# Optimization experiments

Hardware: AMD Instinct MI355X
Metric: run time of the kernel (lower is better)

## Reference

```python
import jax, jax.numpy as jnp
import numpy as np

N_USER = 50000
N_ITEM = 50000
E = 600000
D = 128
H = 2 * D  # FFN hidden
LN_EPS = 1e-5


def _xavier(k, shape):
    lim = float(np.sqrt(6.0 / (shape[0] + shape[1])))
    return jax.random.uniform(k, shape, jnp.float32, -lim, lim)


def setup_inputs() -> dict:
    key = jax.random.key(0)
    ks = jax.random.split(key, 12)
    return {
        "feat_user": jax.random.normal(ks[0], (N_USER, D), jnp.float32),
        "feat_item": jax.random.normal(ks[1], (N_ITEM, D), jnp.float32),
        "W_u2i": _xavier(ks[2], (D, D)),
        "b_u2i": jnp.zeros((D,), jnp.float32),
        "W_i2u": _xavier(ks[3], (D, D)),
        "b_i2u": jnp.zeros((D,), jnp.float32),
        "self_w_user": _xavier(ks[4], (D, D)),
        "self_w_item": _xavier(ks[5], (D, D)),
        "ln_g_user": jnp.ones((D,), jnp.float32),
        "ln_b_user": jnp.zeros((D,), jnp.float32),
        "ln_g_item": jnp.ones((D,), jnp.float32),
        "ln_b_item": jnp.zeros((D,), jnp.float32),
        "ffn_w1": _xavier(ks[6], (D, H)),
        "ffn_b1": jnp.zeros((H,), jnp.float32),
        "ffn_w2": _xavier(ks[7], (H, D)),
        "ffn_b2": jnp.zeros((D,), jnp.float32),
        "src_u2i": jax.random.randint(ks[8], (E,), 0, N_USER, jnp.int32),
        "dst_u2i": jax.random.randint(ks[9], (E,), 0, N_ITEM, jnp.int32),
        "src_i2u": jax.random.randint(ks[10], (E,), 0, N_ITEM, jnp.int32),
        "dst_i2u": jax.random.randint(ks[11], (E,), 0, N_USER, jnp.int32),
    }


def _layer_norm(x, g, b):
    m = jnp.mean(x, axis=-1, keepdims=True)
    v = jnp.mean(jnp.square(x - m), axis=-1, keepdims=True)
    return (x - m) * jax.lax.rsqrt(v + LN_EPS) * g + b


def reference(feat_user, feat_item, W_u2i, b_u2i, W_i2u, b_i2u,
              self_w_user, self_w_item,
              ln_g_user, ln_b_user, ln_g_item, ln_b_item,
              ffn_w1, ffn_b1, ffn_w2, ffn_b2,
              src_u2i, dst_u2i, src_i2u, dst_i2u):
    # GraphConv(norm='none'): transform src feats, gather along edges, sum per dst, add bias.
    msg_item = jax.ops.segment_sum((feat_user @ W_u2i)[src_u2i], dst_u2i,
                                   num_segments=N_ITEM) + b_u2i
    msg_user = jax.ops.segment_sum((feat_item @ W_i2u)[src_i2u], dst_i2u,
                                   num_segments=N_USER) + b_i2u
    # self-loop weight + relation aggregation
    h_user = feat_user @ self_w_user + msg_user
    h_item = feat_item @ self_w_item + msg_item
    # LayerNorm -> ReLU -> residual
    h_user = jax.nn.relu(_layer_norm(h_user, ln_g_user, ln_b_user)) + feat_user
    h_item = jax.nn.relu(_layer_norm(h_item, ln_g_item, ln_b_item)) + feat_item
    # shared FFN (Linear -> ReLU -> Linear)
    def ffn(x):
        return jax.nn.relu(x @ ffn_w1 + ffn_b1) @ ffn_w2 + ffn_b2
    return ffn(h_user), ffn(h_item)
```

## Files before the change

### kernel.cpp

```cpp
#include <hip/hip_runtime.h>

typedef unsigned short u16;
typedef __attribute__((ext_vector_type(4))) float f32x4;
typedef __attribute__((ext_vector_type(8))) short bf16x8;

#define MAXB 512
#define BUK  256
#define EMAX 4096

__device__ __forceinline__ float bf2f(u16 u) {
    union { unsigned int i; float f; } v; v.i = ((unsigned int)u) << 16; return v.f;
}
__device__ __forceinline__ u16 f2bf(float f) {
    union { float f; unsigned int i; } v; v.f = f;
    unsigned int r = v.i + 0x7fffu + ((v.i >> 16) & 1u);
    return (u16)(r >> 16);
}
__device__ __forceinline__ void gload16(const void* g, void* l) {
    __builtin_amdgcn_global_load_lds(
        (const __attribute__((address_space(1))) unsigned int*)g,
        (__attribute__((address_space(3))) unsigned int*)l, 16, 0, 0);
}

#define MFMA_VARS \
    const int tid = threadIdx.x, w = tid >> 6, l = tid & 63; \
    const int wr = (w >> 1) * 64, wc = (w & 1) * 64; \
    const int quad = l >> 4, lan = l & 15; (void)tid;

#define ACC_INIT(A) \
    _Pragma("unroll") for (int i = 0; i < 4; i++) \
    _Pragma("unroll") for (int j = 0; j < 4; j++) A[i][j] = (f32x4){0.f,0.f,0.f,0.f};

#define STAGE_AW(Aptr, sA, Wptr, sW) \
    _Pragma("unroll") for (int it = 0; it < 8; it++) { \
        int o = ((it * 4 + w) * 64 + l) * 16; \
        int row = o >> 8; \
        int sg = ((o >> 4) & 15) ^ (row & 7); \
        gload16((Aptr) + (size_t)row * (sA) + sg * 8, (char*)As + o); \
        gload16((Wptr) + (size_t)row * (sW) + sg * 8, (char*)Ws + o); \
    }

#define STAGE_W(Wptr, sW) \
    _Pragma("unroll") for (int it = 0; it < 8; it++) { \
        int o = ((it * 4 + w) * 64 + l) * 16; \
        int row = o >> 8; \
        int sg = ((o >> 4) & 15) ^ (row & 7); \
        gload16((Wptr) + (size_t)row * (sW) + sg * 8, (char*)Ws + o); \
    }

#define COMPUTE(A) \
    _Pragma("unroll") for (int kk = 0; kk < 4; kk++) { \
        bf16x8 af[4], bfr[4]; \
        _Pragma("unroll") for (int i = 0; i < 4; i++) { \
            int ra = wr + i * 16 + lan; \
            af[i] = *(const bf16x8*)&As[ra * 128 + (((kk * 4 + quad) ^ (ra & 7)) << 3)]; } \
        _Pragma("unroll") for (int j = 0; j < 4; j++) { \
            int rb = wc + j * 16 + lan; \
            bfr[j] = *(const bf16x8*)&Ws[rb * 128 + (((kk * 4 + quad) ^ (rb & 7)) << 3)]; } \
        _Pragma("unroll") for (int i = 0; i < 4; i++) \
        _Pragma("unroll") for (int j = 0; j < 4; j++) \
            A[i][j] = __builtin_amdgcn_mfma_f32_16x16x32_bf16(af[i], bfr[j], A[i][j], 0,0,0); \
    }

__global__ __launch_bounds__(256) void msgln_k(
    const u16* __restrict__ S, u16* __restrict__ fb,
    const u16* __restrict__ wUrel, const u16* __restrict__ wUself,
    const u16* __restrict__ wIrel, const u16* __restrict__ wIself,
    const float* __restrict__ bmU, const float* __restrict__ bmI,
    const float* __restrict__ gU, const float* __restrict__ bU,
    const float* __restrict__ gI, const float* __restrict__ bI,
    int NUp)
{
    __shared__ __align__(16) u16 As[128 * 128];
    __shared__ __align__(16) u16 Ws[128 * 128];
    __shared__ float ps[128][2][2];
    MFMA_VARS
    const int m0 = blockIdx.x * 128;
    const bool isU = m0 < NUp;
    const u16* W0 = isU ? wUrel : wIrel;
    const u16* W1 = isU ? wUself : wIself;
    const float* bm = isU ? bmU : bmI;
    const float* g  = isU ? gU : gI;
    const float* b  = isU ? bU : bI;

    f32x4 acc[4][4];
    ACC_INIT(acc)

    STAGE_AW(S + (size_t)m0 * 128, 128, W0, 128)
    __syncthreads();
    COMPUTE(acc)
    __syncthreads();
    STAGE_AW(fb + (size_t)m0 * 128, 128, W1, 128)
    __syncthreads();
    COMPUTE(acc)

    const int half = wc >> 6;
    float bm4[4], g4[4], b4[4];
#pragma unroll
    for (int j = 0; j < 4; j++) {
        int col = wc + j * 16 + lan;
        bm4[j] = bm[col]; g4[j] = g[col]; b4[j] = b[col];
    }
#pragma unroll
    for (int i = 0; i < 4; i++) {
#pragma unroll
        for (int r = 0; r < 4; r++) {
            float s = 0.f, q = 0.f;
#pragma unroll
            for (int j = 0; j < 4; j++) {
                float v = acc[i][j][r] + bm4[j];
                s += v; q += v * v;
            }
#pragma unroll
            for (int o = 1; o < 16; o <<= 1) {
                s += __shfl_xor(s, o, 64);
                q += __shfl_xor(q, o, 64);
            }
            if (lan == 0) {
                int rl = wr + i * 16 + quad * 4 + r;
                ps[rl][half][0] = s;
                ps[rl][half][1] = q;
            }
        }
    }
    __syncthreads();
#pragma unroll
    for (int i = 0; i < 4; i++) {
#pragma unroll
        for (int r = 0; r < 4; r++) {
            int rl = wr + i * 16 + quad * 4 + r;
            float sum = ps[rl][0][0] + ps[rl][1][0];
            float sq  = ps[rl][0][1] + ps[rl][1][1];
            float mean = sum * 0.0078125f;
            float var  = sq * 0.0078125f - mean * mean;
            float inv  = rsqrtf(var + 1e-5f);
#pragma unroll
            for (int j = 0; j < 4; j++) {
                int col = wc + j * 16 + lan;
                int sgc = ((col >> 3) ^ (rl & 7)) << 3;
                float v = acc[i][j][r] + bm4[j];
                float y = fmaxf(fmaf((v - mean) * inv, g4[j], b4[j]), 0.f)
                          + bf2f(As[rl * 128 + sgc + (col & 7)]);
                fb[(size_t)(m0 + rl) * 128 + col] = f2bf(y);
            }
        }
    }
}

__global__ __launch_bounds__(256) void ffn_k(
    const u16* __restrict__ h, const u16* __restrict__ W1T,
    const float* __restrict__ b1, const u16* __restrict__ W2T,
    const float* __restrict__ b2, float* __restrict__ out,
    int NU, int NUp, int NI)
{
    __shared__ __align__(16) u16 lds[2 * 128 * 128];
    u16* As = lds;
    u16* Ws = lds + 16384;
    MFMA_VARS
    const int m0 = blockIdx.x * 128;

    f32x4 acc1[4][4], acc2[4][4];
    ACC_INIT(acc1)
    ACC_INIT(acc2)

    STAGE_AW(h + (size_t)m0 * 128, 128, W1T, 128)
    __syncthreads();
    COMPUTE(acc1)
    __syncthreads();
    STAGE_W(W1T + (size_t)128 * 128, 128)
    __syncthreads();
    COMPUTE(acc2)
    __syncthreads();

    float b1a[4], b1b[4];
#pragma unroll
    for (int j = 0; j < 4; j++) {
        b1a[j] = b1[wc + j * 16 + lan];
        b1b[j] = b1[128 + wc + j * 16 + lan];
    }
    u16* H = lds;
#pragma unroll
    for (int i = 0; i < 4; i++) {
#pragma unroll
        for (int r = 0; r < 4; r++) {
            int rl = wr + i * 16 + quad * 4 + r;
#pragma unroll
            for (int j = 0; j < 4; j++) {
                int col = wc + j * 16 + lan;
                int gA = col >> 3, od = col & 7;
                H[rl * 256 + ((gA ^ (rl & 7)) << 3) + od] =
                    f2bf(fmaxf(acc1[i][j][r] + b1a[j], 0.f));
                H[rl * 256 + (((16 + gA) ^ (rl & 7)) << 3) + od] =
                    f2bf(fmaxf(acc2[i][j][r] + b1b[j], 0.f));
            }
        }
    }
    __syncthreads();

    f32x4 acc3[4][4];
    ACC_INIT(acc3)
#pragma unroll
    for (int kk = 0; kk < 8; kk++) {
        bf16x8 af[4], bfr[4];
#pragma unroll
        for (int i = 0; i < 4; i++) {
            int ra = wr + i * 16 + lan;
            int lg = kk * 4 + quad;
            af[i] = *(const bf16x8*)&H[ra * 256 + ((lg ^ (ra & 7)) << 3)];
        }
#pragma unroll
        for (int j = 0; j < 4; j++)
            bfr[j] = *(const bf16x8*)&W2T[(size_t)(wc + j * 16 + lan) * 256 + kk * 32 + quad * 8];
#pragma unroll
        for (int i = 0; i < 4; i++)
#pragma unroll
            for (int j = 0; j < 4; j++)
                acc3[i][j] = __builtin_amdgcn_mfma_f32_16x16x32_bf16(af[i], bfr[j], acc3[i][j], 0, 0, 0);
    }

#pragma unroll
    for (int j = 0; j < 4; j++) {
        int col = wc + j * 16 + lan;
        float bb = b2[col];
#pragma unroll
        for (int i = 0; i < 4; i++) {
            int row0 = m0 + wr + i * 16 + quad * 4;
#pragma unroll
            for (int r = 0; r < 4; r++) {
                int gr = row0 + r, orow;
                if (gr < NUp) { if (gr >= NU) continue; orow = gr; }
                else { int ir = gr - NUp; if (ir >= NI) continue; orow = NU + ir; }
                out[(size_t)orow * 128 + col] = acc3[i][j][r] + bb;
            }
        }
    }
}

__global__ __launch_bounds__(256) void prep_k(
    const float* __restrict__ fu, const float* __restrict__ fi,
    u16* __restrict__ fb, u16* __restrict__ S,
    int nu4, int ni4, int NU, int NUp, int NI, int NIp,
    const float* __restrict__ w0, const float* __restrict__ w1,
    const float* __restrict__ w2, const float* __restrict__ w3,
    const float* __restrict__ w4, const float* __restrict__ w5,
    u16* __restrict__ o0, u16* __restrict__ o1, u16* __restrict__ o2,
    u16* __restrict__ o3, u16* __restrict__ o4, u16* __restrict__ o5,
    int* __restrict__ cnt, int NBUK)
{
    int t = blockIdx.x * 256 + threadIdx.x;
    int nc = nu4 + ni4;
    if (t < nc) {
        const float* X; u16* Y; int idx;
        if (t < nu4) { X = fu; Y = fb; idx = t; }
        else { X = fi; Y = fb + (size_t)NUp * 128; idx = t - nu4; }
        float4 v = ((const float4*)X)[idx];
        ((ushort4*)Y)[idx] = make_ushort4(f2bf(v.x), f2bf(v.y), f2bf(v.z), f2bf(v.w));
        return;
    }
    int u = t - nc;
    if (u < 131072) {
        const float* W; u16* O; int K, N, idx;
        if (u < 65536) {
            int s = u >> 14; idx = u & 16383; K = 128; N = 128;
            W = s == 0 ? w0 : s == 1 ? w1 : s == 2 ? w2 : w3;
            O = s == 0 ? o0 : s == 1 ? o1 : s == 2 ? o2 : o3;
        } else {
            int v2 = u - 65536; int s = v2 >> 15; idx = v2 & 32767;
            if (s == 0) { W = w4; O = o4; K = 128; N = 256; }
            else        { W = w5; O = o5; K = 256; N = 128; }
        }
        int k = idx / N, n = idx % N;
        O[n * K + k] = f2bf(W[idx]);
        return;
    }
    int u2 = u - 131072;
    int padrows = (NUp - NU) + (NIp - NI);
    int padw = padrows * 32;
    if (u2 < 2 * padw) {
        int arr = u2 / padw, k = u2 % padw;
        int prow = k >> 5, c4 = k & 31;
        int row = (prow < NUp - NU) ? (NU + prow) : (NUp + NI + (prow - (NUp - NU)));
        u16* B = arr ? fb : S;
        ((ushort4*)B)[(size_t)row * 32 + c4] = make_ushort4(0, 0, 0, 0);
        return;
    }
    int c = u2 - 2 * padw;
    if (c <= NBUK) cnt[c] = 0;
}

__global__ __launch_bounds__(256) void chist_k(
    const int* __restrict__ dst0, const int* __restrict__ dst1,
    int* __restrict__ cnt, int E, int NI, int NBUK)
{
    __shared__ int lh[MAXB];
    int t = threadIdx.x;
    for (int i = t; i < MAXB; i += 256) lh[i] = 0;
    __syncthreads();
    for (long long e = (long long)blockIdx.x * 256 + t; e < 2LL * E;
         e += (long long)gridDim.x * 256) {
        int row = (e < E) ? dst0[e] : NI + dst1[e - E];
        atomicAdd(&lh[row >> 8], 1);
    }
    __syncthreads();
    for (int i = t; i < NBUK; i += 256)
        if (lh[i]) atomicAdd(&cnt[i], lh[i]);
}

__global__ __launch_bounds__(512) void cscan_k(
    const int* __restrict__ cnt, int* __restrict__ crp, int* __restrict__ chead,
    int* __restrict__ rowptr, int NBUK, int NR)
{
    __shared__ int s[512];
    int t = threadIdx.x;
    int carry = 0;
    for (int base = 0; base < NBUK; base += 512) {
        int i = base + t;
        int v = (i < NBUK) ? cnt[i] : 0;
        s[t] = v;
        __syncthreads();
        for (int off = 1; off < 512; off <<= 1) {
            int x = (t >= off) ? s[t - off] : 0;
            __syncthreads();
            s[t] += x;
            __syncthreads();
        }
        int excl = s[t] - v + carry;
        if (i < NBUK) { crp[i] = excl; chead[i] = excl; }
        carry += s[511];
        __syncthreads();
    }
    if (t == 0) { crp[NBUK] = carry; rowptr[NR] = carry; }
}

__global__ __launch_bounds__(256) void cpart_k(
    const int* __restrict__ src0, const int* __restrict__ dst0,
    const int* __restrict__ src1, const int* __restrict__ dst1,
    int* __restrict__ chead, unsigned int* __restrict__ ebuf,
    int E, int NI, int NBUK)
{
    __shared__ int lh[MAXB], lb[MAXB], lo[MAXB];
    int t = threadIdx.x;
    long long total = 2LL * E;
    long long per = (total + gridDim.x - 1) / gridDim.x;
    long long r0 = (long long)blockIdx.x * per;
    long long r1 = r0 + per; if (r1 > total) r1 = total;

    for (int i = t; i < MAXB; i += 256) { lh[i] = 0; lo[i] = 0; }
    __syncthreads();
    for (long long e = r0 + t; e < r1; e += 256) {
        int row = (e < E) ? dst0[e] : NI + dst1[e - E];
        atomicAdd(&lh[row >> 8], 1);
    }
    __syncthreads();
    for (int i = t; i < NBUK; i += 256)
        if (lh[i]) lb[i] = atomicAdd(&chead[i], lh[i]);
    __syncthreads();
    for (long long e = r0 + t; e < r1; e += 256) {
        int row, src;
        if (e < E) { row = dst0[e]; src = src0[e]; }
        else       { row = NI + dst1[e - E]; src = src1[e - E]; }
        int bin = row >> 8;
        int off = atomicAdd(&lo[bin], 1);
        ebuf[lb[bin] + off] = ((unsigned int)(row & 255) << 16) | (unsigned int)src;
    }
}

__global__ __launch_bounds__(256) void fsort_k(
    const int* __restrict__ crp, const unsigned int* __restrict__ ebuf,
    int* __restrict__ rowptr, u16* __restrict__ eidx, int NR)
{
    __shared__ unsigned int ep[EMAX];
    __shared__ u16 ss[EMAX];
    __shared__ int h[BUK], hd[BUK];
    int b = blockIdx.x, t = threadIdx.x;
    int base = crp[b];
    int n = crp[b + 1] - base;
    if (n > EMAX) n = EMAX;

    for (int i = t; i < n; i += 256) ep[i] = ebuf[base + i];
    if (t < BUK) h[t] = 0;
    __syncthreads();
    for (int i = t; i < n; i += 256) atomicAdd(&h[ep[i] >> 16], 1);
    __syncthreads();
    int v = (t < BUK) ? h[t] : 0;
    for (int off = 1; off < 256; off <<= 1) {
        int x = (t >= off) ? h[t - off] : 0;
        __syncthreads();
        if (t < BUK) h[t] += x;
        __syncthreads();
    }
    int excl = (t < BUK) ? (h[t] - v) : 0;
    if (t < BUK) {
        int absrow = b * BUK + t;
        if (absrow < NR) rowptr[absrow] = base + excl;
        hd[t] = excl;
    }
    __syncthreads();
    for (int i = t; i < n; i += 256) {
        unsigned int p = ep[i];
        int pos = atomicAdd(&hd[p >> 16], 1);
        ss[pos] = (u16)(p & 0xffffu);
    }
    __syncthreads();
    for (int i = t; i < n; i += 256) eidx[base + i] = ss[i];
}

__global__ __launch_bounds__(256) void gather_k(
    const int* __restrict__ rowptr, const u16* __restrict__ eidx,
    const u16* __restrict__ fb, u16* __restrict__ S,
    int NI, int NR, int NUp)
{
    int row = blockIdx.x * 4 + (threadIdx.x >> 6);
    int l = threadIdx.x & 63;
    if (row >= NR) return;
    const u16* F = (row < NI) ? fb : fb + (size_t)NUp * 128;
    int srow = (row < NI) ? (NUp + row) : (row - NI);
    int start = rowptr[row], end = rowptr[row + 1];
    int sub = l >> 4, li = l & 15;

    float a[8];
#pragma unroll
    for (int k = 0; k < 8; k++) a[k] = 0.f;

    for (int j = start; j < end; j += 16) {
        int idx[4]; uint4 v[4];
#pragma unroll
        for (int u = 0; u < 4; u++) {
            int je = j + u * 4 + sub;
            int c = je < end ? je : end - 1;
            idx[u] = eidx[c];
        }
#pragma unroll
        for (int u = 0; u < 4; u++)
            v[u] = *(const uint4*)(F + (size_t)idx[u] * 128 + li * 8);
#pragma unroll
        for (int u = 0; u < 4; u++) {
            if (j + u * 4 + sub < end) {
                unsigned int ww[4] = {v[u].x, v[u].y, v[u].z, v[u].w};
#pragma unroll
                for (int p = 0; p < 4; p++) {
                    a[2*p]   += bf2f((u16)(ww[p] & 0xffffu));
                    a[2*p+1] += bf2f((u16)(ww[p] >> 16));
                }
            }
        }
    }
#pragma unroll
    for (int k = 0; k < 8; k++) {
        a[k] += __shfl_xor(a[k], 16, 64);
        a[k] += __shfl_xor(a[k], 32, 64);
    }
    if (sub == 0) {
        uint4 o;
        o.x = ((unsigned int)f2bf(a[1]) << 16) | f2bf(a[0]);
        o.y = ((unsigned int)f2bf(a[3]) << 16) | f2bf(a[2]);
        o.z = ((unsigned int)f2bf(a[5]) << 16) | f2bf(a[4]);
        o.w = ((unsigned int)f2bf(a[7]) << 16) | f2bf(a[6]);
        *(uint4*)(S + (size_t)srow * 128 + li * 8) = o;
    }
}

extern "C" void kernel_launch(void* const* d_in, const int* in_sizes, int n_in,
                              void* d_out, int out_size, void* d_ws, size_t ws_size,
                              hipStream_t stream)
{
    const float* feat_user   = (const float*)d_in[0];
    const float* feat_item   = (const float*)d_in[1];
    const float* W_u2i       = (const float*)d_in[2];
    const float* b_u2i       = (const float*)d_in[3];
    const float* W_i2u       = (const float*)d_in[4];
    const float* b_i2u       = (const float*)d_in[5];
    const float* self_w_user = (const float*)d_in[6];
    const float* self_w_item = (const float*)d_in[7];
    const float* ln_g_user   = (const float*)d_in[8];
    const float* ln_b_user   = (const float*)d_in[9];
    const float* ln_g_item   = (const float*)d_in[10];
    const float* ln_b_item   = (const float*)d_in[11];
    const float* ffn_w1      = (const float*)d_in[12];
    const float* ffn_b1      = (const float*)d_in[13];
    const float* ffn_w2      = (const float*)d_in[14];
    const float* ffn_b2      = (const float*)d_in[15];
    const int* src_u2i       = (const int*)d_in[16];
    const int* dst_u2i       = (const int*)d_in[17];
    const int* src_i2u       = (const int*)d_in[18];
    const int* dst_i2u       = (const int*)d_in[19];

    const int NU = in_sizes[0] / 128;
    const int NI = in_sizes[1] / 128;
    const int E  = in_sizes[16];
    const int NR = NI + NU;
    const int NUp = (NU + 127) & ~127;
    const int NIp = (NI + 127) & ~127;
    const int NRp = NUp + NIp;
    const int NBUK = (NR + BUK - 1) / BUK;

    char* ws = (char*)d_ws;
    u16* S  = (u16*)ws;
    u16* fb = S + (size_t)NRp * 128;
    char* R2 = (char*)(fb + (size_t)NRp * 128);

    int* cnt    = (int*)R2;
    int* crp    = cnt + (NBUK + 1);
    int* chead  = crp + (NBUK + 1);
    int* rowptr = chead + NBUK;
    unsigned int* ebuf = (unsigned int*)(rowptr + NR + 1);
    u16* eidx   = (u16*)(ebuf + 2 * (size_t)E);
    u16* wts    = (u16*)(eidx + 2 * (size_t)E);
    u16* w_u2iT = wts;
    u16* w_i2uT = w_u2iT + 16384;
    u16* selfUT = w_i2uT + 16384;
    u16* selfIT = selfUT + 16384;
    u16* ffn1T  = selfIT + 16384;
    u16* ffn2T  = ffn1T + 32768;

    float* out = (float*)d_out;
    dim3 blk(256);
    const int nu4 = NU * 128 / 4, ni4 = NI * 128 / 4;
    const int padw = ((NUp - NU) + (NIp - NI)) * 32;
    const int prep_n = nu4 + ni4 + 131072 + 2 * padw + NBUK + 1;

    prep_k<<<dim3((prep_n + 255) / 256), blk, 0, stream>>>(
        feat_user, feat_item, fb, S, nu4, ni4, NU, NUp, NI, NIp,
        W_u2i, W_i2u, self_w_user, self_w_item, ffn_w1, ffn_w2,
        w_u2iT, w_i2uT, selfUT, selfIT, ffn1T, ffn2T, cnt, NBUK);

    chist_k<<<dim3(512), blk, 0, stream>>>(dst_u2i, dst_i2u, cnt, E, NI, NBUK);
    cscan_k<<<dim3(1), dim3(512), 0, stream>>>(cnt, crp, chead, rowptr, NBUK, NR);
    cpart_k<<<dim3(512), blk, 0, stream>>>(
        src_u2i, dst_u2i, src_i2u, dst_i2u, chead, ebuf, E, NI, NBUK);
    fsort_k<<<dim3(NBUK), blk, 0, stream>>>(crp, ebuf, rowptr, eidx, NR);

    gather_k<<<dim3((NR + 3) / 4), blk, 0, stream>>>(
        rowptr, eidx, fb, S, NI, NR, NUp);

    msgln_k<<<dim3(NRp / 128), blk, 0, stream>>>(
        S, fb, w_i2uT, selfUT, w_u2iT, selfIT,
        b_i2u, b_u2i, ln_g_user, ln_b_user, ln_g_item, ln_b_item, NUp);

    ffn_k<<<dim3(NRp / 128), blk, 0, stream>>>(
        fb, ffn1T, ffn_b1, ffn2T, ffn_b2, out, NU, NUp, NI);
}
```

Measured before the change: 301.6 us.

## Read weights from global in GEMMs and chunk FFN hidden to cut LDS and registers

```diff
diff --git a/kernel.cpp b/kernel.cpp
--- a/kernel.cpp
+++ b/kernel.cpp
@@ -31,32 +31,22 @@
     _Pragma("unroll") for (int i = 0; i < 4; i++) \
     _Pragma("unroll") for (int j = 0; j < 4; j++) A[i][j] = (f32x4){0.f,0.f,0.f,0.f};
 
-#define STAGE_AW(Aptr, sA, Wptr, sW) \
+#define STAGE_A(Aptr, sA) \
     _Pragma("unroll") for (int it = 0; it < 8; it++) { \
         int o = ((it * 4 + w) * 64 + l) * 16; \
         int row = o >> 8; \
         int sg = ((o >> 4) & 15) ^ (row & 7); \
         gload16((Aptr) + (size_t)row * (sA) + sg * 8, (char*)As + o); \
-        gload16((Wptr) + (size_t)row * (sW) + sg * 8, (char*)Ws + o); \
-    }
-
-#define STAGE_W(Wptr, sW) \
-    _Pragma("unroll") for (int it = 0; it < 8; it++) { \
-        int o = ((it * 4 + w) * 64 + l) * 16; \
-        int row = o >> 8; \
-        int sg = ((o >> 4) & 15) ^ (row & 7); \
-        gload16((Wptr) + (size_t)row * (sW) + sg * 8, (char*)Ws + o); \
-    }
-
-#define COMPUTE(A) \
+    }
+
+#define COMPUTE_BG(A, Wg, sW) \
     _Pragma("unroll") for (int kk = 0; kk < 4; kk++) { \
         bf16x8 af[4], bfr[4]; \
+        _Pragma("unroll") for (int j = 0; j < 4; j++) \
+            bfr[j] = *(const bf16x8*)&(Wg)[(size_t)(wc + j*16 + lan) * (sW) + kk*32 + quad*8]; \
         _Pragma("unroll") for (int i = 0; i < 4; i++) { \
             int ra = wr + i * 16 + lan; \
             af[i] = *(const bf16x8*)&As[ra * 128 + (((kk * 4 + quad) ^ (ra & 7)) << 3)]; } \
-        _Pragma("unroll") for (int j = 0; j < 4; j++) { \
-            int rb = wc + j * 16 + lan; \
-            bfr[j] = *(const bf16x8*)&Ws[rb * 128 + (((kk * 4 + quad) ^ (rb & 7)) << 3)]; } \
         _Pragma("unroll") for (int i = 0; i < 4; i++) \
         _Pragma("unroll") for (int j = 0; j < 4; j++) \
             A[i][j] = __builtin_amdgcn_mfma_f32_16x16x32_bf16(af[i], bfr[j], A[i][j], 0,0,0); \
@@ -72,7 +62,6 @@
     int NUp)
 {
     __shared__ __align__(16) u16 As[128 * 128];
-    __shared__ __align__(16) u16 Ws[128 * 128];
     __shared__ float ps[128][2][2];
     MFMA_VARS
     const int m0 = blockIdx.x * 128;
@@ -86,13 +75,13 @@
     f32x4 acc[4][4];
     ACC_INIT(acc)
 
-    STAGE_AW(S + (size_t)m0 * 128, 128, W0, 128)
-    __syncthreads();
-    COMPUTE(acc)
-    __syncthreads();
-    STAGE_AW(fb + (size_t)m0 * 128, 128, W1, 128)
-    __syncthreads();
-    COMPUTE(acc)
+    STAGE_A(S + (size_t)m0 * 128, 128)
+    __syncthreads();
+    COMPUTE_BG(acc, W0, 128)
+    __syncthreads();
+    STAGE_A(fb + (size_t)m0 * 128, 128)
+    __syncthreads();
+    COMPUTE_BG(acc, W1, 128)
 
     const int half = wc >> 6;
     float bm4[4], g4[4], b4[4];
@@ -153,69 +142,77 @@
     const float* __restrict__ b2, float* __restrict__ out,
     int NU, int NUp, int NI)
 {
-    __shared__ __align__(16) u16 lds[2 * 128 * 128];
-    u16* As = lds;
-    u16* Ws = lds + 16384;
+    __shared__ __align__(16) u16 As[128 * 128];
+    __shared__ __align__(16) u16 Hq[128 * 64];
     MFMA_VARS
     const int m0 = blockIdx.x * 128;
 
-    f32x4 acc1[4][4], acc2[4][4];
-    ACC_INIT(acc1)
-    ACC_INIT(acc2)
-
-    STAGE_AW(h + (size_t)m0 * 128, 128, W1T, 128)
-    __syncthreads();
-    COMPUTE(acc1)
-    __syncthreads();
-    STAGE_W(W1T + (size_t)128 * 128, 128)
-    __syncthreads();
-    COMPUTE(acc2)
-    __syncthreads();
-
-    float b1a[4], b1b[4];
-#pragma unroll
-    for (int j = 0; j < 4; j++) {
-        b1a[j] = b1[wc + j * 16 + lan];
-        b1b[j] = b1[128 + wc + j * 16 + lan];
-    }
-    u16* H = lds;
-#pragma unroll
-    for (int i = 0; i < 4; i++) {
-#pragma unroll
-        for (int r = 0; r < 4; r++) {
-            int rl = wr + i * 16 + quad * 4 + r;
-#pragma unroll
-            for (int j = 0; j < 4; j++) {
-                int col = wc + j * 16 + lan;
-                int gA = col >> 3, od = col & 7;
-                H[rl * 256 + ((gA ^ (rl & 7)) << 3) + od] =
-                    f2bf(fmaxf(acc1[i][j][r] + b1a[j], 0.f));
-                H[rl * 256 + (((16 + gA) ^ (rl & 7)) << 3) + od] =
-                    f2bf(fmaxf(acc2[i][j][r] + b1b[j], 0.f));
-            }
-        }
-    }
-    __syncthreads();
-
     f32x4 acc3[4][4];
     ACC_INIT(acc3)
-#pragma unroll
-    for (int kk = 0; kk < 8; kk++) {
-        bf16x8 af[4], bfr[4];
-#pragma unroll
-        for (int i = 0; i < 4; i++) {
-            int ra = wr + i * 16 + lan;
-            int lg = kk * 4 + quad;
-            af[i] = *(const bf16x8*)&H[ra * 256 + ((lg ^ (ra & 7)) << 3)];
-        }
-#pragma unroll
-        for (int j = 0; j < 4; j++)
-            bfr[j] = *(const bf16x8*)&W2T[(size_t)(wc + j * 16 + lan) * 256 + kk * 32 + quad * 8];
-#pragma unroll
-        for (int i = 0; i < 4; i++)
+
+    STAGE_A(h + (size_t)m0 * 128, 128)
+    __syncthreads();
+
+    const int rb = w * 32;
+    for (int q = 0; q < 4; q++) {
+        f32x4 aq[2][4];
+#pragma unroll
+        for (int i = 0; i < 2; i++)
+#pragma unroll
+            for (int j = 0; j < 4; j++) aq[i][j] = (f32x4){0.f, 0.f, 0.f, 0.f};
+#pragma unroll
+        for (int kk = 0; kk < 4; kk++) {
+            bf16x8 af[2], bfr[4];
 #pragma unroll
             for (int j = 0; j < 4; j++)
-                acc3[i][j] = __builtin_amdgcn_mfma_f32_16x16x32_bf16(af[i], bfr[j], acc3[i][j], 0, 0, 0);
+                bfr[j] = *(const bf16x8*)&W1T[(size_t)(q * 64 + j * 16 + lan) * 128 + kk * 32 + quad * 8];
+#pragma unroll
+            for (int i = 0; i < 2; i++) {
+                int ra = rb + i * 16 + lan;
+                af[i] = *(const bf16x8*)&As[ra * 128 + (((kk * 4 + quad) ^ (ra & 7)) << 3)];
+            }
+#pragma unroll
+            for (int i = 0; i < 2; i++)
+#pragma unroll
+                for (int j = 0; j < 4; j++)
+                    aq[i][j] = __builtin_amdgcn_mfma_f32_16x16x32_bf16(af[i], bfr[j], aq[i][j], 0, 0, 0);
+        }
+        float b1v[4];
+#pragma unroll
+        for (int j = 0; j < 4; j++) b1v[j] = b1[q * 64 + j * 16 + lan];
+
+        __syncthreads();
+#pragma unroll
+        for (int i = 0; i < 2; i++) {
+#pragma unroll
+            for (int r = 0; r < 4; r++) {
+                int rl = rb + i * 16 + quad * 4 + r;
+#pragma unroll
+                for (int j = 0; j < 4; j++) {
+                    int cq = j * 16 + lan;
+                    Hq[rl * 64 + (((cq >> 3) ^ (rl & 7)) << 3) + (cq & 7)] =
+                        f2bf(fmaxf(aq[i][j][r] + b1v[j], 0.f));
+                }
+            }
+        }
+        __syncthreads();
+#pragma unroll
+        for (int kk = 0; kk < 2; kk++) {
+            bf16x8 af[4], bfr[4];
+#pragma unroll
+            for (int j = 0; j < 4; j++)
+                bfr[j] = *(const bf16x8*)&W2T[(size_t)(wc + j * 16 + lan) * 256 + q * 64 + kk * 32 + quad * 8];
+#pragma unroll
+            for (int i = 0; i < 4; i++) {
+                int ra = wr + i * 16 + lan;
+                af[i] = *(const bf16x8*)&Hq[ra * 64 + (((kk * 4 + quad) ^ (ra & 7)) << 3)];
+            }
+#pragma unroll
+            for (int i = 0; i < 4; i++)
+#pragma unroll
+                for (int j = 0; j < 4; j++)
+                    acc3[i][j] = __builtin_amdgcn_mfma_f32_16x16x32_bf16(af[i], bfr[j], acc3[i][j], 0, 0, 0);
+        }
     }
 
 #pragma unroll
```

New measurement: 358.6 us. 1.19x slower.
